# Optimization experiments

Hardware: AMD Instinct MI355X
Metric: run time of the kernel (lower is better)

## Reference

```python
import jax, jax.numpy as jnp
import numpy as np

N_NODES = 100000
N_EDGES = 6400000
NUM_TYPES = 4
AVG_NUM_NEIGHBORS = 64.0


def setup_inputs() -> dict:
    key = jax.random.key(0)
    k1, k2, k3 = jax.random.split(key, 3)
    edge_eng = jax.random.normal(k1, (N_EDGES, 1), dtype=jnp.float32)
    edge_index = jax.random.randint(k2, (2, N_EDGES), 0, N_NODES, dtype=jnp.int64)
    species = jax.random.randint(k3, (N_NODES, 1), 0, NUM_TYPES, dtype=jnp.int64)
    per_edge_scales = jnp.ones((NUM_TYPES, NUM_TYPES), dtype=jnp.float32)
    return {"edge_eng": edge_eng, "edge_index": edge_index, "species": species,
            "per_edge_scales": per_edge_scales}


def reference(edge_eng, edge_index, species, per_edge_scales):
    # edge_eng: [E,1], edge_index: [2,E], species: [N,1], per_edge_scales: [T,T]
    edge_center = edge_index[0]
    edge_neighbor = edge_index[1]
    sp = species[:, 0]                      # [N]
    center_species = sp[edge_center]        # [E]
    neighbor_species = sp[edge_neighbor]    # [E]
    scale = per_edge_scales[center_species, neighbor_species]  # [E]
    e = edge_eng * scale[:, None]           # [E,1]
    atom_eng = jax.ops.segment_sum(e, edge_center, num_segments=sp.shape[0])  # [N,1]
    factor = 1.0 / np.sqrt(AVG_NUM_NEIGHBORS)
    return atom_eng * jnp.float32(factor)
```

## Files before the change

kernel.cpp:

```cpp
#include <hip/hip_runtime.h>


#define BUCKET_SHIFT 10
#define BUCKET_NODES 1024
#define STAGE_NB     104
#define CAP          80
#define STR          81
#define K1_THREADS   512
#define CHUNK        4096
#define NSTRIPE      8
#define MAX_SP_WORDS 6272
#define OVF_CAP      8192

__global__ void k0_pack(const int* __restrict__ species,
                        unsigned int* __restrict__ packed,
                        int* __restrict__ ovf_cnt,
                        int n_nodes, int n_words)
{
    const int w = blockIdx.x * blockDim.x + threadIdx.x;
    if (w == 0) *ovf_cnt = 0;
    if (w >= n_words) return;
    const int base = w * 16;
    unsigned int v = 0;
    if (base + 16 <= n_nodes) {
#pragma unroll
        for (int q = 0; q < 4; ++q) {
            const int4 s4 = *(const int4*)(species + base + 4 * q);
            v |= (unsigned int)(s4.x & 3) << (8 * q + 0);
            v |= (unsigned int)(s4.y & 3) << (8 * q + 2);
            v |= (unsigned int)(s4.z & 3) << (8 * q + 4);
            v |= (unsigned int)(s4.w & 3) << (8 * q + 6);
        }
    } else {
        const int m = n_nodes - base;
        for (int j = 0; j < m; ++j)
            v |= (unsigned int)(species[base + j] & 3) << (2 * j);
    }
    packed[w] = v;
}

__global__ void __launch_bounds__(K1_THREADS)
k1_scatter(const float* __restrict__ edge_eng,
           const int*   __restrict__ edge_center,
           const int*   __restrict__ edge_neighbor,
           const unsigned int* __restrict__ sp_packed,
           const float* __restrict__ scales,
           unsigned int* __restrict__ recs,
           int*          __restrict__ cnts,
           int2*         __restrict__ ovf,
           int*          __restrict__ ovf_cnt,
           int n_edges, int nb, int n_sp_words)
{
    __shared__ unsigned int s_sp[MAX_SP_WORDS];
    __shared__ unsigned int stage[STAGE_NB * STR];
    __shared__ float s_scale[16];
    __shared__ int cursor[STAGE_NB];

    const int tid = threadIdx.x;
    if (tid < 16) s_scale[tid] = scales[tid] * 0.125f;
    for (int i = tid; i < n_sp_words; i += K1_THREADS) s_sp[i] = sp_packed[i];
    for (int b = tid; b < nb; b += K1_THREADS) cursor[b] = 0;
    __syncthreads();

    const int cid = blockIdx.x;
    const int lo  = cid * CHUNK;

    int4   c4[2];
    int4   n4[2];
    float4 e4[2];
    const bool full = ((n_edges & 3) == 0) && (lo + CHUNK <= n_edges);
    if (full) {
#pragma unroll
        for (int k = 0; k < 2; ++k) {
            const int idx = lo + 4 * tid + (4 * K1_THREADS) * k;
            c4[k] = *(const int4*)  (edge_center   + idx);
            n4[k] = *(const int4*)  (edge_neighbor + idx);
            e4[k] = *(const float4*)(edge_eng      + idx);
        }
    } else {
#pragma unroll
        for (int k = 0; k < 2; ++k) {
            const int idx = lo + 4 * tid + (4 * K1_THREADS) * k;
            int*   cp = (int*)  &c4[k];
            int*   np = (int*)  &n4[k];
            float* ep = (float*)&e4[k];
#pragma unroll
            for (int j = 0; j < 4; ++j) {
                const int i = idx + j;
                if (i < n_edges) { cp[j] = edge_center[i]; np[j] = edge_neighbor[i]; ep[j] = edge_eng[i]; }
                else             { cp[j] = -1; np[j] = 0; ep[j] = 0.0f; }
            }
        }
    }

#define SP(n) ((s_sp[(unsigned)(n) >> 4] >> (((n) & 15) << 1)) & 3)
#pragma unroll
    for (int k = 0; k < 2; ++k) {
        const int*   cp = (const int*)  &c4[k];
        const int*   np = (const int*)  &n4[k];
        const float* ep = (const float*)&e4[k];
#pragma unroll
        for (int j = 0; j < 4; ++j) {
            const int c = cp[j];
            if (c < 0) continue;
            const int   b = c >> BUCKET_SHIFT;
            const float v = ep[j] * s_scale[(SP(c) << 2) | SP(np[j])];
            const unsigned int rec = (__float_as_uint(v) & 0xFFFFFC00u)
                                   | ((unsigned int)c & (BUCKET_NODES - 1));
            const int r = atomicAdd(&cursor[b], 1);
            if (r < CAP) {
                stage[b * STR + r] = rec;
            } else {
                const int oi = atomicAdd(ovf_cnt, 1);
                if (oi < OVF_CAP) ovf[oi] = make_int2(c, __float_as_int(v));
            }
        }
    }
#undef SP
    __syncthreads();

    const int wav  = tid >> 6;
    const int lane = tid & 63;
    for (int b = wav; b < nb; b += (K1_THREADS / 64)) {
        const int cnt = min(cursor[b], CAP);
        unsigned int* dst = recs + ((size_t)cid * nb + b) * CAP;
        for (int i = lane; i < cnt; i += 64) dst[i] = stage[b * STR + i];
        if (lane == 0) cnts[cid * nb + b] = cnt;
    }
}

__global__ void k2_accumulate(const unsigned int* __restrict__ recs,
                              const int*  __restrict__ cnts,
                              float*      __restrict__ partials,
                              int n_chunks, int nb)
{
    __shared__ float acc[BUCKET_NODES];
    __shared__ int s_cnt[256];
    const int b    = blockIdx.x / NSTRIPE;
    const int s    = blockIdx.x % NSTRIPE;
    const int tid  = threadIdx.x;
    const int lane = tid & 63;
    const int wav  = tid >> 6;

    const int nseg = (n_chunks - s + NSTRIPE - 1) / NSTRIPE;

    for (int i = tid; i < BUCKET_NODES; i += blockDim.x) acc[i] = 0.0f;
    for (int t = tid; t < nseg; t += blockDim.x) {
        const int cid = s + NSTRIPE * t;
        s_cnt[t] = cnts[cid * nb + b];
    }
    __syncthreads();

    for (int t = wav; t < nseg; t += 4) {
        const int cid = s + NSTRIPE * t;
        const int cnt = s_cnt[t];
        const unsigned int* p = recs + ((size_t)cid * nb + b) * CAP;
        for (int i = lane; i < cnt; i += 64) {
            const unsigned int r = p[i];
            atomicAdd(&acc[r & (BUCKET_NODES - 1)],
                      __uint_as_float(r & 0xFFFFFC00u));
        }
    }
    __syncthreads();

    float* dst = partials + (size_t)blockIdx.x * BUCKET_NODES;
    for (int i = tid; i < BUCKET_NODES; i += blockDim.x) dst[i] = acc[i];
}

__global__ void k3_reduce(const float* __restrict__ partials,
                          float*       __restrict__ out, int n_nodes)
{
    const int n = blockIdx.x * blockDim.x + threadIdx.x;
    if (n >= n_nodes) return;
    const int b     = n >> BUCKET_SHIFT;
    const int local = n & (BUCKET_NODES - 1);
    const float* p  = partials + (size_t)b * NSTRIPE * BUCKET_NODES + local;
    float sum = 0.0f;
#pragma unroll
    for (int i = 0; i < NSTRIPE; ++i) sum += p[i * BUCKET_NODES];
    out[n] = sum;
}

__global__ void k4_overflow(const int2* __restrict__ ovf,
                            const int*  __restrict__ ovf_cnt,
                            float*      __restrict__ out)
{
    const int n = min(*ovf_cnt, OVF_CAP);
    for (int i = threadIdx.x; i < n; i += blockDim.x)
        atomicAdd(&out[ovf[i].x], __int_as_float(ovf[i].y));
}

__global__ void fallback_atomic_kernel(const float* __restrict__ edge_eng,
                                       const int*   __restrict__ edge_center,
                                       const int*   __restrict__ edge_neighbor,
                                       const int*   __restrict__ species,
                                       const float* __restrict__ scales,
                                       float*       __restrict__ out, int n_edges)
{
    __shared__ float s_scale[16];
    if (threadIdx.x < 16) s_scale[threadIdx.x] = scales[threadIdx.x] * 0.125f;
    __syncthreads();
    const int stride = gridDim.x * blockDim.x;
    for (int i = blockIdx.x * blockDim.x + threadIdx.x; i < n_edges; i += stride) {
        const int c  = edge_center[i];
        const int cs = species[c];
        const int ns = species[edge_neighbor[i]];
        atomicAdd(&out[c], edge_eng[i] * s_scale[(cs << 2) | ns]);
    }
}

extern "C" void kernel_launch(void* const* d_in, const int* in_sizes, int n_in,
                              void* d_out, int out_size, void* d_ws, size_t ws_size,
                              hipStream_t stream) {
    const float* edge_eng   = (const float*)d_in[0];
    const int*   edge_index = (const int*)  d_in[1];
    const int*   species    = (const int*)  d_in[2];
    const float* scales     = (const float*)d_in[3];
    float*       out        = (float*)      d_out;

    const int n_edges = in_sizes[1] / 2;
    const int n_nodes = in_sizes[2];
    const int* edge_center   = edge_index;
    const int* edge_neighbor = edge_index + n_edges;

    const int nb       = (n_nodes + BUCKET_NODES - 1) >> BUCKET_SHIFT;
    const int n_words  = (n_nodes + 15) / 16;
    const int n_chunks = (n_edges + CHUNK - 1) / CHUNK;

    const size_t off_ovfcnt   = 0;
    const size_t off_packed   = 4096;
    const size_t off_recs     = (off_packed + (size_t)n_words * 4 + 255) & ~(size_t)255;
    const size_t off_cnts     = off_recs + (size_t)n_chunks * nb * CAP * 4;
    const size_t off_partials = (off_cnts + (size_t)n_chunks * nb * 4 + 255) & ~(size_t)255;
    const size_t off_ovf      = off_partials + (size_t)nb * NSTRIPE * BUCKET_NODES * 4;
    const size_t needed       = off_ovf + (size_t)OVF_CAP * sizeof(int2);

    if (nb > STAGE_NB || n_words > MAX_SP_WORDS ||
        (n_chunks + NSTRIPE - 1) / NSTRIPE > 256 ||
        ws_size < needed) {
        hipMemsetAsync(d_out, 0, (size_t)out_size * sizeof(float), stream);
        int grid = (n_edges + 255) / 256;
        if (grid > 2048) grid = 2048;
        fallback_atomic_kernel<<<grid, 256, 0, stream>>>(
            edge_eng, edge_center, edge_neighbor, species, scales, out, n_edges);
        return;
    }

    int*          ovf_cnt  = (int*)         ((char*)d_ws + off_ovfcnt);
    unsigned int* packed   = (unsigned int*)((char*)d_ws + off_packed);
    unsigned int* recs     = (unsigned int*)((char*)d_ws + off_recs);
    int*          cnts     = (int*)         ((char*)d_ws + off_cnts);
    float*        partials = (float*)       ((char*)d_ws + off_partials);
    int2*         ovf      = (int2*)        ((char*)d_ws + off_ovf);

    k0_pack<<<(n_words + 255) / 256, 256, 0, stream>>>(
        species, packed, ovf_cnt, n_nodes, n_words);

    k1_scatter<<<n_chunks, K1_THREADS, 0, stream>>>(
        edge_eng, edge_center, edge_neighbor, packed, scales,
        recs, cnts, ovf, ovf_cnt, n_edges, nb, n_words);

    k2_accumulate<<<nb * NSTRIPE, 256, 0, stream>>>(recs, cnts, partials, n_chunks, nb);

    k3_reduce<<<(n_nodes + 255) / 256, 256, 0, stream>>>(partials, out, n_nodes);

    k4_overflow<<<1, 256, 0, stream>>>(ovf, ovf_cnt, out);
}
```

Baseline: 88.84 us.

## Compact scatter records per bucket-stripe with global atomic cursors

The scatter kernel now reserves space in one contiguous per-(bucket, stripe) record array through a global atomicAdd, instead of writing fixed-capacity per-chunk slots with separate counts. The accumulate kernel can then read dense, vectorized uint4 records, and each bucket-stripe is split across two blocks of 512 threads. This removes the padded sparse slot layout and the per-chunk count loop in the accumulate pass. In exchange it adds global atomics per chunk and bucket, doubles the number of partials the reduce pass sums, and sends records past the fixed capacity into the overflow path.

```diff
diff --git a/kernel.cpp b/kernel.cpp
--- a/kernel.cpp
+++ b/kernel.cpp
@@ -9,16 +9,21 @@
 #define K1_THREADS   512
 #define CHUNK        4096
 #define NSTRIPE      8
+#define CAP8         9216
+#define KSPLIT       2
+#define K2_THREADS   512
 #define MAX_SP_WORDS 6272
 #define OVF_CAP      8192
 
 __global__ void k0_pack(const int* __restrict__ species,
                         unsigned int* __restrict__ packed,
                         int* __restrict__ ovf_cnt,
-                        int n_nodes, int n_words)
+                        int* __restrict__ gcnt,
+                        int n_nodes, int n_words, int n_cnt)
 {
     const int w = blockIdx.x * blockDim.x + threadIdx.x;
     if (w == 0) *ovf_cnt = 0;
+    if (w < n_cnt) gcnt[w] = 0;
     if (w >= n_words) return;
     const int base = w * 16;
     unsigned int v = 0;
@@ -46,7 +51,7 @@
            const unsigned int* __restrict__ sp_packed,
            const float* __restrict__ scales,
            unsigned int* __restrict__ recs,
-           int*          __restrict__ cnts,
+           int*          __restrict__ gcnt,
            int2*         __restrict__ ovf,
            int*          __restrict__ ovf_cnt,
            int n_edges, int nb, int n_sp_words)
@@ -55,6 +60,7 @@
     __shared__ unsigned int stage[STAGE_NB * STR];
     __shared__ float s_scale[16];
     __shared__ int cursor[STAGE_NB];
+    __shared__ int rbase[STAGE_NB];
 
     const int tid = threadIdx.x;
     if (tid < 16) s_scale[tid] = scales[tid] * 0.125f;
@@ -62,8 +68,9 @@
     for (int b = tid; b < nb; b += K1_THREADS) cursor[b] = 0;
     __syncthreads();
 
-    const int cid = blockIdx.x;
-    const int lo  = cid * CHUNK;
+    const int cid    = blockIdx.x;
+    const int stripe = cid & (NSTRIPE - 1);
+    const int lo     = cid * CHUNK;
 
     int4   c4[2];
     int4   n4[2];
@@ -119,52 +126,70 @@
 #undef SP
     __syncthreads();
 
+    for (int b = tid; b < nb; b += K1_THREADS) {
+        const int cnt = min(cursor[b], CAP);
+        rbase[b] = cnt ? atomicAdd(&gcnt[(b << 3) | stripe], cnt) : 0;
+    }
+    __syncthreads();
+
     const int wav  = tid >> 6;
     const int lane = tid & 63;
     for (int b = wav; b < nb; b += (K1_THREADS / 64)) {
-        const int cnt = min(cursor[b], CAP);
-        unsigned int* dst = recs + ((size_t)cid * nb + b) * CAP;
-        for (int i = lane; i < cnt; i += 64) dst[i] = stage[b * STR + i];
-        if (lane == 0) cnts[cid * nb + b] = cnt;
-    }
-}
-
-__global__ void k2_accumulate(const unsigned int* __restrict__ recs,
-                              const int*  __restrict__ cnts,
-                              float*      __restrict__ partials,
-                              int n_chunks, int nb)
+        const int cnt  = min(cursor[b], CAP);
+        const int base = rbase[b];
+        unsigned int* dst = recs + (size_t)((b << 3) | stripe) * CAP8;
+        for (int i = lane; i < cnt; i += 64) {
+            const int pos = base + i;
+            const unsigned int rec = stage[b * STR + i];
+            if (pos < CAP8) {
+                dst[pos] = rec;
+            } else {
+                const int oi = atomicAdd(ovf_cnt, 1);
+                if (oi < OVF_CAP)
+                    ovf[oi] = make_int2((b << BUCKET_SHIFT) | (int)(rec & (BUCKET_NODES - 1)),
+                                        __float_as_int(__uint_as_float(rec & 0xFFFFFC00u)));
+            }
+        }
+    }
+}
+
+__global__ void __launch_bounds__(K2_THREADS)
+k2_accumulate(const unsigned int* __restrict__ recs,
+              const int*  __restrict__ gcnt,
+              float*      __restrict__ partials)
 {
     __shared__ float acc[BUCKET_NODES];
-    __shared__ int s_cnt[256];
-    const int b    = blockIdx.x / NSTRIPE;
-    const int s    = blockIdx.x % NSTRIPE;
-    const int tid  = threadIdx.x;
-    const int lane = tid & 63;
-    const int wav  = tid >> 6;
-
-    const int nseg = (n_chunks - s + NSTRIPE - 1) / NSTRIPE;
-
-    for (int i = tid; i < BUCKET_NODES; i += blockDim.x) acc[i] = 0.0f;
-    for (int t = tid; t < nseg; t += blockDim.x) {
-        const int cid = s + NSTRIPE * t;
-        s_cnt[t] = cnts[cid * nb + b];
-    }
-    __syncthreads();
-
-    for (int t = wav; t < nseg; t += 4) {
-        const int cid = s + NSTRIPE * t;
-        const int cnt = s_cnt[t];
-        const unsigned int* p = recs + ((size_t)cid * nb + b) * CAP;
-        for (int i = lane; i < cnt; i += 64) {
-            const unsigned int r = p[i];
-            atomicAdd(&acc[r & (BUCKET_NODES - 1)],
-                      __uint_as_float(r & 0xFFFFFC00u));
-        }
+    const int bs  = blockIdx.x / KSPLIT;
+    const int s   = blockIdx.x % KSPLIT;
+    const int tid = threadIdx.x;
+
+    for (int i = tid; i < BUCKET_NODES; i += K2_THREADS) acc[i] = 0.0f;
+    __syncthreads();
+
+    const int count = min(gcnt[bs], CAP8);
+    const int lo = (int)(((long long)count * s / KSPLIT)) & ~15;
+    const int hi = (s == KSPLIT - 1) ? count
+                                     : ((int)(((long long)count * (s + 1) / KSPLIT)) & ~15);
+    const unsigned int* p = recs + (size_t)bs * CAP8;
+
+    const int hiv = hi & ~3;
+    for (int i = lo + 4 * tid; i + 4 <= hiv + 4; i += 4 * K2_THREADS) {
+        if (i + 4 <= hiv) {
+            const uint4 r = *(const uint4*)(p + i);
+            atomicAdd(&acc[r.x & (BUCKET_NODES - 1)], __uint_as_float(r.x & 0xFFFFFC00u));
+            atomicAdd(&acc[r.y & (BUCKET_NODES - 1)], __uint_as_float(r.y & 0xFFFFFC00u));
+            atomicAdd(&acc[r.z & (BUCKET_NODES - 1)], __uint_as_float(r.z & 0xFFFFFC00u));
+            atomicAdd(&acc[r.w & (BUCKET_NODES - 1)], __uint_as_float(r.w & 0xFFFFFC00u));
+        }
+    }
+    for (int i = hiv + tid; i < hi; i += K2_THREADS) {
+        const unsigned int r = p[i];
+        atomicAdd(&acc[r & (BUCKET_NODES - 1)], __uint_as_float(r & 0xFFFFFC00u));
     }
     __syncthreads();
 
     float* dst = partials + (size_t)blockIdx.x * BUCKET_NODES;
-    for (int i = tid; i < BUCKET_NODES; i += blockDim.x) dst[i] = acc[i];
+    for (int i = tid; i < BUCKET_NODES; i += K2_THREADS) dst[i] = acc[i];
 }
 
 __global__ void k3_reduce(const float* __restrict__ partials,
@@ -174,10 +199,10 @@
     if (n >= n_nodes) return;
     const int b     = n >> BUCKET_SHIFT;
     const int local = n & (BUCKET_NODES - 1);
-    const float* p  = partials + (size_t)b * NSTRIPE * BUCKET_NODES + local;
+    const float* p  = partials + (size_t)b * NSTRIPE * KSPLIT * BUCKET_NODES + local;
     float sum = 0.0f;
 #pragma unroll
-    for (int i = 0; i < NSTRIPE; ++i) sum += p[i * BUCKET_NODES];
+    for (int i = 0; i < NSTRIPE * KSPLIT; ++i) sum += p[i * BUCKET_NODES];
     out[n] = sum;
 }
 
@@ -226,18 +251,17 @@
     const int nb       = (n_nodes + BUCKET_NODES - 1) >> BUCKET_SHIFT;
     const int n_words  = (n_nodes + 15) / 16;
     const int n_chunks = (n_edges + CHUNK - 1) / CHUNK;
+    const int n_cnt    = nb * NSTRIPE;
 
     const size_t off_ovfcnt   = 0;
-    const size_t off_packed   = 4096;
+    const size_t off_gcnt     = 256;
+    const size_t off_packed   = (off_gcnt + (size_t)n_cnt * 4 + 255) & ~(size_t)255;
     const size_t off_recs     = (off_packed + (size_t)n_words * 4 + 255) & ~(size_t)255;
-    const size_t off_cnts     = off_recs + (size_t)n_chunks * nb * CAP * 4;
-    const size_t off_partials = (off_cnts + (size_t)n_chunks * nb * 4 + 255) & ~(size_t)255;
-    const size_t off_ovf      = off_partials + (size_t)nb * NSTRIPE * BUCKET_NODES * 4;
+    const size_t off_partials = off_recs + (size_t)n_cnt * CAP8 * 4;
+    const size_t off_ovf      = off_partials + (size_t)n_cnt * KSPLIT * BUCKET_NODES * 4;
     const size_t needed       = off_ovf + (size_t)OVF_CAP * sizeof(int2);
 
-    if (nb > STAGE_NB || n_words > MAX_SP_WORDS ||
-        (n_chunks + NSTRIPE - 1) / NSTRIPE > 256 ||
-        ws_size < needed) {
+    if (nb > STAGE_NB || n_words > MAX_SP_WORDS || ws_size < needed) {
         hipMemsetAsync(d_out, 0, (size_t)out_size * sizeof(float), stream);
         int grid = (n_edges + 255) / 256;
         if (grid > 2048) grid = 2048;
@@ -247,20 +271,20 @@
     }
 
     int*          ovf_cnt  = (int*)         ((char*)d_ws + off_ovfcnt);
+    int*          gcnt     = (int*)         ((char*)d_ws + off_gcnt);
     unsigned int* packed   = (unsigned int*)((char*)d_ws + off_packed);
     unsigned int* recs     = (unsigned int*)((char*)d_ws + off_recs);
-    int*          cnts     = (int*)         ((char*)d_ws + off_cnts);
     float*        partials = (float*)       ((char*)d_ws + off_partials);
     int2*         ovf      = (int2*)        ((char*)d_ws + off_ovf);
 
     k0_pack<<<(n_words + 255) / 256, 256, 0, stream>>>(
-        species, packed, ovf_cnt, n_nodes, n_words);
+        species, packed, ovf_cnt, gcnt, n_nodes, n_words, n_cnt);
 
     k1_scatter<<<n_chunks, K1_THREADS, 0, stream>>>(
         edge_eng, edge_center, edge_neighbor, packed, scales,
-        recs, cnts, ovf, ovf_cnt, n_edges, nb, n_words);
-
-    k2_accumulate<<<nb * NSTRIPE, 256, 0, stream>>>(recs, cnts, partials, n_chunks, nb);
+        recs, gcnt, ovf, ovf_cnt, n_edges, nb, n_words);
+
+    k2_accumulate<<<n_cnt * KSPLIT, K2_THREADS, 0, stream>>>(recs, gcnt, partials);
 
     k3_reduce<<<(n_nodes + 255) / 256, 256, 0, stream>>>(partials, out, n_nodes);
 
```

Result: slower. 98.35 us (+10.7%).

## Zero-pad bucket records and store bucket-major for flat vectorized accumulation

Applied to the files above, without the earlier changes.

The scatter kernel now zero-fills its shared staging buffer and always writes all CAP slots per bucket, laid out bucket-major instead of chunk-major. Unused slots decode as +0.0 added to node 0 of the bucket, so the per-chunk counts array goes away. The accumulate kernel then streams each bucket's contiguous record region with uint4 loads, split over 16 blocks of 512 threads instead of 8 blocks of 256. This gives coalesced, count-free reads and more parallelism, at the cost of writing and reading padding slots (about 64 of 80 used on average) and extra shared-atomic traffic on slot 0 from those zeros.

```diff
diff --git a/kernel.cpp b/kernel.cpp
--- a/kernel.cpp
+++ b/kernel.cpp
@@ -8,7 +8,8 @@
 #define STR          81
 #define K1_THREADS   512
 #define CHUNK        4096
-#define NSTRIPE      8
+#define KS           16
+#define K2_THREADS   512
 #define MAX_SP_WORDS 6272
 #define OVF_CAP      8192
 
@@ -46,10 +47,9 @@
            const unsigned int* __restrict__ sp_packed,
            const float* __restrict__ scales,
            unsigned int* __restrict__ recs,
-           int*          __restrict__ cnts,
            int2*         __restrict__ ovf,
            int*          __restrict__ ovf_cnt,
-           int n_edges, int nb, int n_sp_words)
+           int n_edges, int n_chunks, int nb, int n_sp_words)
 {
     __shared__ unsigned int s_sp[MAX_SP_WORDS];
     __shared__ unsigned int stage[STAGE_NB * STR];
@@ -59,6 +59,7 @@
     const int tid = threadIdx.x;
     if (tid < 16) s_scale[tid] = scales[tid] * 0.125f;
     for (int i = tid; i < n_sp_words; i += K1_THREADS) s_sp[i] = sp_packed[i];
+    for (int i = tid; i < nb * STR; i += K1_THREADS) stage[i] = 0u;
     for (int b = tid; b < nb; b += K1_THREADS) cursor[b] = 0;
     __syncthreads();
 
@@ -122,49 +123,40 @@
     const int wav  = tid >> 6;
     const int lane = tid & 63;
     for (int b = wav; b < nb; b += (K1_THREADS / 64)) {
-        const int cnt = min(cursor[b], CAP);
-        unsigned int* dst = recs + ((size_t)cid * nb + b) * CAP;
-        for (int i = lane; i < cnt; i += 64) dst[i] = stage[b * STR + i];
-        if (lane == 0) cnts[cid * nb + b] = cnt;
-    }
-}
-
-__global__ void k2_accumulate(const unsigned int* __restrict__ recs,
-                              const int*  __restrict__ cnts,
-                              float*      __restrict__ partials,
-                              int n_chunks, int nb)
+        unsigned int* dst = recs + ((size_t)b * n_chunks + cid) * CAP;
+#pragma unroll
+        for (int i = lane; i < CAP; i += 64)
+            dst[i] = stage[b * STR + i];
+    }
+}
+
+__global__ void __launch_bounds__(K2_THREADS)
+k2_accumulate(const unsigned int* __restrict__ recs,
+              float* __restrict__ partials,
+              int n_chunks)
 {
     __shared__ float acc[BUCKET_NODES];
-    __shared__ int s_cnt[256];
-    const int b    = blockIdx.x / NSTRIPE;
-    const int s    = blockIdx.x % NSTRIPE;
-    const int tid  = threadIdx.x;
-    const int lane = tid & 63;
-    const int wav  = tid >> 6;
-
-    const int nseg = (n_chunks - s + NSTRIPE - 1) / NSTRIPE;
-
-    for (int i = tid; i < BUCKET_NODES; i += blockDim.x) acc[i] = 0.0f;
-    for (int t = tid; t < nseg; t += blockDim.x) {
-        const int cid = s + NSTRIPE * t;
-        s_cnt[t] = cnts[cid * nb + b];
-    }
-    __syncthreads();
-
-    for (int t = wav; t < nseg; t += 4) {
-        const int cid = s + NSTRIPE * t;
-        const int cnt = s_cnt[t];
-        const unsigned int* p = recs + ((size_t)cid * nb + b) * CAP;
-        for (int i = lane; i < cnt; i += 64) {
-            const unsigned int r = p[i];
-            atomicAdd(&acc[r & (BUCKET_NODES - 1)],
-                      __uint_as_float(r & 0xFFFFFC00u));
-        }
+    const int b   = blockIdx.x / KS;
+    const int s   = blockIdx.x % KS;
+    const int tid = threadIdx.x;
+
+    for (int i = tid; i < BUCKET_NODES; i += K2_THREADS) acc[i] = 0.0f;
+    __syncthreads();
+
+    const unsigned int* p = recs + (size_t)b * n_chunks * CAP;
+    const int total = n_chunks * CAP;
+
+    for (int i = (s * K2_THREADS + tid) * 4; i + 4 <= total; i += KS * K2_THREADS * 4) {
+        const uint4 r = *(const uint4*)(p + i);
+        atomicAdd(&acc[r.x & (BUCKET_NODES - 1)], __uint_as_float(r.x & 0xFFFFFC00u));
+        atomicAdd(&acc[r.y & (BUCKET_NODES - 1)], __uint_as_float(r.y & 0xFFFFFC00u));
+        atomicAdd(&acc[r.z & (BUCKET_NODES - 1)], __uint_as_float(r.z & 0xFFFFFC00u));
+        atomicAdd(&acc[r.w & (BUCKET_NODES - 1)], __uint_as_float(r.w & 0xFFFFFC00u));
     }
     __syncthreads();
 
     float* dst = partials + (size_t)blockIdx.x * BUCKET_NODES;
-    for (int i = tid; i < BUCKET_NODES; i += blockDim.x) dst[i] = acc[i];
+    for (int i = tid; i < BUCKET_NODES; i += K2_THREADS) dst[i] = acc[i];
 }
 
 __global__ void k3_reduce(const float* __restrict__ partials,
@@ -174,10 +166,10 @@
     if (n >= n_nodes) return;
     const int b     = n >> BUCKET_SHIFT;
     const int local = n & (BUCKET_NODES - 1);
-    const float* p  = partials + (size_t)b * NSTRIPE * BUCKET_NODES + local;
+    const float* p  = partials + (size_t)b * KS * BUCKET_NODES + local;
     float sum = 0.0f;
 #pragma unroll
-    for (int i = 0; i < NSTRIPE; ++i) sum += p[i * BUCKET_NODES];
+    for (int i = 0; i < KS; ++i) sum += p[i * BUCKET_NODES];
     out[n] = sum;
 }
 
@@ -230,14 +222,11 @@
     const size_t off_ovfcnt   = 0;
     const size_t off_packed   = 4096;
     const size_t off_recs     = (off_packed + (size_t)n_words * 4 + 255) & ~(size_t)255;
-    const size_t off_cnts     = off_recs + (size_t)n_chunks * nb * CAP * 4;
-    const size_t off_partials = (off_cnts + (size_t)n_chunks * nb * 4 + 255) & ~(size_t)255;
-    const size_t off_ovf      = off_partials + (size_t)nb * NSTRIPE * BUCKET_NODES * 4;
+    const size_t off_partials = off_recs + (size_t)nb * n_chunks * CAP * 4;
+    const size_t off_ovf      = off_partials + (size_t)nb * KS * BUCKET_NODES * 4;
     const size_t needed       = off_ovf + (size_t)OVF_CAP * sizeof(int2);
 
-    if (nb > STAGE_NB || n_words > MAX_SP_WORDS ||
-        (n_chunks + NSTRIPE - 1) / NSTRIPE > 256 ||
-        ws_size < needed) {
+    if (nb > STAGE_NB || n_words > MAX_SP_WORDS || ws_size < needed) {
         hipMemsetAsync(d_out, 0, (size_t)out_size * sizeof(float), stream);
         int grid = (n_edges + 255) / 256;
         if (grid > 2048) grid = 2048;
@@ -249,7 +238,6 @@
     int*          ovf_cnt  = (int*)         ((char*)d_ws + off_ovfcnt);
     unsigned int* packed   = (unsigned int*)((char*)d_ws + off_packed);
     unsigned int* recs     = (unsigned int*)((char*)d_ws + off_recs);
-    int*          cnts     = (int*)         ((char*)d_ws + off_cnts);
     float*        partials = (float*)       ((char*)d_ws + off_partials);
     int2*         ovf      = (int2*)        ((char*)d_ws + off_ovf);
 
@@ -258,9 +246,9 @@
 
     k1_scatter<<<n_chunks, K1_THREADS, 0, stream>>>(
         edge_eng, edge_center, edge_neighbor, packed, scales,
-        recs, cnts, ovf, ovf_cnt, n_edges, nb, n_words);
-
-    k2_accumulate<<<nb * NSTRIPE, 256, 0, stream>>>(recs, cnts, partials, n_chunks, nb);
+        recs, ovf, ovf_cnt, n_edges, n_chunks, nb, n_words);
+
+    k2_accumulate<<<nb * KS, K2_THREADS, 0, stream>>>(recs, partials, n_chunks);
 
     k3_reduce<<<(n_nodes + 255) / 256, 256, 0, stream>>>(partials, out, n_nodes);
 
```

Measured after the change: 130.9 us. 1.47x slower.
